# Kernel tuning notes

Hardware: AMD Instinct MI355X
Metric: run time of the kernel (lower is better)

Reference implementation:

```python
import jax, jax.numpy as jnp
import numpy as np

B, N, DPOS, F, P, K = 32, 1024, 3, 64, 128, 16


def setup_inputs() -> dict:
    key = jax.random.key(0)
    kp, kf, kw1, kw2 = jax.random.split(key, 4)
    points = jax.random.normal(kp, (B, N, DPOS), dtype=jnp.float32)
    features = jax.random.normal(kf, (B, N, F), dtype=jnp.float32)
    W1 = jax.random.normal(kw1, (2 * F, 2 * P), dtype=jnp.float32) * (1.0 / np.sqrt(2 * F))
    b1 = jnp.zeros((2 * P,), dtype=jnp.float32)
    W2 = jax.random.normal(kw2, (2 * P, P), dtype=jnp.float32) * (1.0 / np.sqrt(2 * P))
    b2 = jnp.zeros((P,), dtype=jnp.float32)
    return {"points": points, "features": features, "W1": W1, "b1": b1, "W2": W2, "b2": b2}


def reference(points, features, W1, b1, W2, b2):
    # pairwise squared distances: r_i - 2 p_i.p_j + r_j + 1e-5  -> [B, N, N]
    r = jnp.sum(points * points, axis=2, keepdims=True)
    m = jnp.einsum('bnd,bmd->bnm', points, points)
    D = r - 2.0 * m + jnp.swapaxes(r, 1, 2) + 1e-5
    # K+1 nearest (incl. self), drop self -> indices [B, N, K]
    _, idx = jax.lax.top_k(-D, K + 1)
    idx = idx[:, :, 1:]
    # gather neighbor features: [B, N, K, F]
    neighbors = features[jnp.arange(B)[:, None, None], idx]
    center = jnp.broadcast_to(features[:, :, None, :], neighbors.shape)
    local = jnp.concatenate([neighbors - center, center], axis=-1)  # [B,N,K,2F]
    # 2-layer MLP with exact GELU
    h = jax.nn.gelu(jnp.einsum('bnkf,fh->bnkh', local, W1) + b1, approximate=False)
    out = jax.nn.gelu(jnp.einsum('bnkh,hp->bnkp', h, W2) + b2, approximate=False)
    # mean over neighbors -> [B, N, P]
    return jnp.mean(out, axis=2)
```

## Files before the change

kernel.cpp:

```cpp
#include <hip/hip_runtime.h>
#include <math.h>

#define BB 32
#define NN 1024
#define FF 64
#define PP 128
#define KNN 16
#define H2 256
#define F2 128
#define KSEL 17
#define SVCAP 272

typedef float f32x4 __attribute__((ext_vector_type(4)));
typedef _Float16 f16x8 __attribute__((ext_vector_type(8)));

#define GC1 0.39616247f
#define GC3 -0.05891477f
#define GC5 0.00563735f
#define GC7 -2.10439e-4f
#define GXC 3.2988f

__device__ __forceinline__ float gelu_poly(float x) {
    float xc = __builtin_amdgcn_fmed3f(x, -GXC, GXC);
    float s = xc * xc;
    float t = fmaf(s, GC7, GC5);
    t = fmaf(s, t, GC3);
    t = fmaf(s, t, GC1);
    float u = fmaf(xc, t, 0.5f);
    return x * u;
}

__device__ __forceinline__ f16x8 splat8(float f) {
    _Float16 h = (_Float16)f;
    f16x8 v = {h, h, h, h, h, h, h, h};
    return v;
}

__device__ __forceinline__ f16x8 act8(f16x8 gv, f16x8 qv) {
    const f16x8 XL = splat8(-GXC), XH = splat8(GXC);
    const f16x8 C1 = splat8(GC1), C3 = splat8(GC3), C5 = splat8(GC5), C7 = splat8(GC7);
    const f16x8 HF = splat8(0.5f);
    f16x8 x  = gv + qv;
    f16x8 xc = __builtin_elementwise_min(__builtin_elementwise_max(x, XL), XH);
    f16x8 s  = xc * xc;
    f16x8 t  = s * C7 + C5;
    t = s * t + C3;
    t = s * t + C1;
    f16x8 u = xc * t + HF;
    return x * u;
}

__global__ __launch_bounds__(512, 8) void knn_prep(const float* __restrict__ points,
                                                   int* __restrict__ idx_out,
                                                   const float* __restrict__ W1,
                                                   const float* __restrict__ W2,
                                                   _Float16* __restrict__ Wcf,
                                                   _Float16* __restrict__ W2f) {
    if (blockIdx.x >= 4096) {
        int tid = (blockIdx.x - 4096) * 512 + threadIdx.x;
        if (tid < 4096) {
            const int lane = tid & 63, quad = lane >> 4, l16 = lane & 15;
            const int kk = (tid >> 6) & 1, n_tile = tid >> 7;
            const int n = n_tile * 16 + l16;
            const int kb = kk * 32 + quad * 8;
            f16x8 v;
#pragma unroll
            for (int j = 0; j < 8; ++j) {
                const int k = kb + j;
                float x = (n < 256) ? W1[k * 256 + n]
                                    : (W1[(64 + k) * 256 + (n - 256)] - W1[k * 256 + (n - 256)]);
                v[j] = (_Float16)x;
            }
            *(f16x8*)(Wcf + (size_t)tid * 8) = v;
        } else {
            const int t2 = tid - 4096;
            const int lane = t2 & 63, quad = lane >> 4, l16 = lane & 15;
            const int nt = (t2 >> 6) & 7, kk8 = t2 >> 9;
            const int p = nt * 16 + l16;
            const int hb = kk8 * 32 + quad * 8;
            f16x8 v;
#pragma unroll
            for (int j = 0; j < 8; ++j) v[j] = (_Float16)W2[(size_t)(hb + j) * PP + p];
            *(f16x8*)(W2f + (size_t)t2 * 8) = v;
        }
        return;
    }

    __shared__ float px[NN], py[NN], pz[NN], rr[NN];
    __shared__ unsigned sv_val[8][SVCAP];
    __shared__ unsigned sv_idx[8][SVCAP];
    __shared__ unsigned tie_idx[8][64];

    const int t = threadIdx.x;
    const int w = t >> 6, lane = t & 63;
    const int b = blockIdx.x >> 7;
    const int q0 = (blockIdx.x & 127) * 8;
    const float* pb = points + (size_t)b * NN * 3;
    const unsigned long long lt = (1ull << lane) - 1ull;

    for (int i = t; i < NN; i += 512) {
        float x = pb[3 * i], y = pb[3 * i + 1], z = pb[3 * i + 2];
        px[i] = x; py[i] = y; pz[i] = z;
        rr[i] = __fadd_rn(__fadd_rn(__fmul_rn(x, x), __fmul_rn(y, y)), __fmul_rn(z, z));
    }
    __syncthreads();

    const int qn = q0 + w;
    const int gq = b * NN + qn;
    const float qx = px[qn], qy = py[qn], qz = pz[qn], qw = rr[qn];

    float D[16];
#pragma unroll
    for (int j = 0; j < 16; ++j) {
        const int m = j * 64 + lane;
        float dot = __fadd_rn(__fadd_rn(__fmul_rn(qx, px[m]), __fmul_rn(qy, py[m])),
                              __fmul_rn(qz, pz[m]));
        D[j] = __fadd_rn(__fadd_rn(__fsub_rn(qw, __fmul_rn(2.0f, dot)), rr[m]), 1e-5f);
    }

    float mnf = D[0];
#pragma unroll
    for (int j = 1; j < 16; ++j) mnf = fminf(mnf, D[j]);
    const unsigned mbits = __float_as_uint(mnf);

    const unsigned mhi = mbits >> 16;
    unsigned Thi = 0;
#pragma unroll
    for (int bit = 15; bit >= 0; --bit) {
        unsigned cand = Thi | (1u << bit);
        int cnt = __popcll(__ballot(mhi < cand));
        if (cnt < KSEL) Thi = cand;
    }
    const unsigned T = (Thi << 16) | 0xFFFFu;

    unsigned base = 0;
#pragma unroll
    for (int j = 0; j < 16; ++j) {
        unsigned vb = __float_as_uint(D[j]);
        bool keep = (vb <= T);
        unsigned long long m = __ballot(keep);
        if (keep) {
            unsigned pos = base + (unsigned)__popcll(m & lt);
            if (pos < SVCAP) { sv_val[w][pos] = vb; sv_idx[w][pos] = j * 64 + lane; }
        }
        base += (unsigned)__popcll(m);
    }
    unsigned C = base > SVCAP ? SVCAP : base;
    const int S = (int)((C + 63) >> 6);

    unsigned Ts = 0;
    if (S == 1) {
        unsigned xv0 = (lane < (int)C) ? sv_val[w][lane] : 0xFFFFFFFFu;
#pragma unroll
        for (int bit = 31; bit >= 0; --bit) {
            unsigned cand = Ts | (1u << bit);
            int cnt = __popcll(__ballot(xv0 < cand));
            if (cnt < KSEL) Ts = cand;
        }
    } else {
        for (int bit = 31; bit >= 0; --bit) {
            unsigned cand = Ts | (1u << bit);
            int cnt = 0;
            for (int s = 0; s < S; ++s) {
                int i = s * 64 + lane;
                unsigned vb = (i < (int)C) ? sv_val[w][i] : 0xFFFFFFFFu;
                cnt += __popcll(__ballot(vb < cand));
            }
            if (cnt < KSEL) Ts = cand;
        }
    }

    int L = 0;
    for (int s = 0; s < S; ++s) {
        int i = s * 64 + lane;
        unsigned vb = (i < (int)C) ? sv_val[w][i] : 0xFFFFFFFFu;
        L += __popcll(__ballot(vb < Ts));
    }
    const int need = KSEL - L;

    unsigned vmin_l = 0xFFFFFFFFu;
    for (int s = 0; s < S; ++s) {
        int i = s * 64 + lane;
        unsigned vb = (i < (int)C) ? sv_val[w][i] : 0xFFFFFFFFu;
        vmin_l = vmin_l < vb ? vmin_l : vb;
    }
#pragma unroll
    for (int off = 32; off >= 1; off >>= 1) {
        unsigned o2 = __shfl_xor(vmin_l, off, 64);
        vmin_l = vmin_l < o2 ? vmin_l : o2;
    }
    const unsigned Vmin = vmin_l;
    unsigned imin_l = 0xFFFFFFFFu;
    for (int s = 0; s < S; ++s) {
        int i = s * 64 + lane;
        unsigned vb = (i < (int)C) ? sv_val[w][i] : 0xFFFFFFFFu;
        unsigned mi = (i < (int)C) ? sv_idx[w][i] : 0xFFFFFFFFu;
        if (vb == Vmin && mi < imin_l) imin_l = mi;
    }
#pragma unroll
    for (int off = 32; off >= 1; off >>= 1) {
        unsigned o2 = __shfl_xor(imin_l, off, 64);
        imin_l = imin_l < o2 ? imin_l : o2;
    }
    const unsigned dropIdx = imin_l;

    int* o = idx_out + (size_t)gq * KNN;
    unsigned wbase = 0, tbase = 0;
    for (int s = 0; s < S; ++s) {
        int i = s * 64 + lane;
        unsigned vb = (i < (int)C) ? sv_val[w][i] : 0xFFFFFFFFu;
        unsigned mi = (i < (int)C) ? sv_idx[w][i] : 0xFFFFFFFFu;
        bool wk = (vb < Ts) && (mi != dropIdx);
        unsigned long long wm = __ballot(wk);
        if (wk) o[wbase + (unsigned)__popcll(wm & lt)] = (int)mi;
        wbase += (unsigned)__popcll(wm);
        bool tk = (vb == Ts);
        unsigned long long tm2 = __ballot(tk);
        if (tk) {
            unsigned tp = tbase + (unsigned)__popcll(tm2 & lt);
            if (tp < 64) tie_idx[w][tp] = mi;
        }
        tbase += (unsigned)__popcll(tm2);
    }
    unsigned tc = tbase > 64 ? 64 : tbase;
    if ((int)tc == need) {
        bool tk = (lane < (int)tc);
        unsigned mi2 = tk ? tie_idx[w][lane] : 0xFFFFFFFFu;
        tk = tk && (mi2 != dropIdx);
        unsigned long long m3 = __ballot(tk);
        if (tk) o[wbase + (unsigned)__popcll(m3 & lt)] = (int)mi2;
    } else if (lane == 0) {
        unsigned pos = wbase;
        for (int r = 0; r < need; ++r) {
            unsigned best = 0xFFFFFFFFu; int bj = 0;
            for (int j2 = 0; j2 < (int)tc; ++j2) {
                unsigned mi = tie_idx[w][j2];
                if (mi < best) { best = mi; bj = j2; }
            }
            tie_idx[w][bj] = 0xFFFFFFFFu;
            if (best != dropIdx) o[pos++] = (int)best;
        }
    }
}

__global__ __launch_bounds__(256, 4) void gq_gemm(const float* __restrict__ feat,
                                                  const _Float16* __restrict__ Wcf,
                                                  const float* __restrict__ b1,
                                                  _Float16* __restrict__ Gall,
                                                  _Float16* __restrict__ Qall) {
    __shared__ __align__(16) _Float16 st[4][16][136];
    const int t = threadIdx.x, w = t >> 6, lane = t & 63;
    const int quad = lane >> 4, l16 = lane & 15;
    const int m0 = blockIdx.x * 16;

    f16x8 a[2];
#pragma unroll
    for (int kk = 0; kk < 2; ++kk) {
        const float* ap = feat + (size_t)(m0 + l16) * 64 + kk * 32 + quad * 8;
        float4 a0 = *(const float4*)ap, a1 = *(const float4*)(ap + 4);
        f16x8 v;
        v[0] = (_Float16)a0.x; v[1] = (_Float16)a0.y; v[2] = (_Float16)a0.z; v[3] = (_Float16)a0.w;
        v[4] = (_Float16)a1.x; v[5] = (_Float16)a1.y; v[6] = (_Float16)a1.z; v[7] = (_Float16)a1.w;
        a[kk] = v;
    }
    f32x4 acc[8];
#pragma unroll
    for (int nt = 0; nt < 8; ++nt) acc[nt] = (f32x4){0.f, 0.f, 0.f, 0.f};
#pragma unroll
    for (int kk = 0; kk < 2; ++kk)
#pragma unroll
        for (int nt = 0; nt < 8; ++nt) {
            f16x8 bf = *(const f16x8*)(Wcf + (size_t)(((w * 8 + nt) * 2 + kk) * 64 + lane) * 8);
            acc[nt] = __builtin_amdgcn_mfma_f32_16x16x32_f16(a[kk], bf, acc[nt], 0, 0, 0);
        }

    const bool isQ = (w >= 2);
#pragma unroll
    for (int nt = 0; nt < 8; ++nt) {
        const int col = nt * 16 + l16;
        const float bias = isQ ? b1[(w - 2) * 128 + col] : 0.f;
#pragma unroll
        for (int r = 0; r < 4; ++r)
            st[w][quad * 4 + r][col] = (_Float16)(acc[nt][r] + bias);
    }
    __syncthreads();

    const int row = lane >> 2, c = lane & 3;
    const int m = m0 + row;
#pragma unroll
    for (int i = 0; i < 4; ++i) {
        const int col = c * 32 + i * 8;
        f16x8 v = *(const f16x8*)&st[w][row][col];
        if (!isQ) *(f16x8*)(Gall + (size_t)m * H2 + w * 128 + col) = v;
        else      *(f16x8*)(Qall + (size_t)m * H2 + (w - 2) * 128 + col) = v;
    }
}

__global__ __launch_bounds__(512, 4) void fused_mlp10(const _Float16* __restrict__ Gall,
                                                      const _Float16* __restrict__ Qall,
                                                      const int* __restrict__ knn_idx,
                                                      const _Float16* __restrict__ W2f,
                                                      const float* __restrict__ b2,
                                                      float* __restrict__ out) {
    __shared__ __align__(16) _Float16 w2s[16384];
    const int t = threadIdx.x, w = t >> 6, lane = t & 63;
    const int quad = lane >> 4, l16 = lane & 15;

    const int lb = ((blockIdx.x & 7) << 8) | (blockIdx.x >> 3);

    const int q0 = (lb * 8 + w) * 2;
    const int b = q0 >> 10;
    const int nb0 = knn_idx[q0 * KNN + l16];
    const int nb1 = knn_idx[(q0 + 1) * KNN + l16];
    const _Float16* g0 = Gall + ((size_t)(b << 10) + nb0) * H2;
    const _Float16* g1 = Gall + ((size_t)(b << 10) + nb1) * H2;
    const _Float16* qq0 = Qall + (size_t)q0 * H2;
    const _Float16* qq1 = qq0 + H2;

    f32x4 acc[2][8];
#pragma unroll
    for (int tm = 0; tm < 2; ++tm)
#pragma unroll
        for (int nt = 0; nt < 8; ++nt) acc[tm][nt] = (f32x4){0.f, 0.f, 0.f, 0.f};

#pragma unroll
    for (int h = 0; h < 2; ++h) {
        if (h) __syncthreads();
#pragma unroll
        for (int i = 0; i < 4; ++i) {
            f16x8 v = *(const f16x8*)(W2f + (size_t)(h * 16384 + i * 4096 + t * 8));
            *(f16x8*)&w2s[i * 4096 + t * 8] = v;
        }
        __syncthreads();

#pragma unroll
        for (int ql = 0; ql < 2; ++ql)
#pragma unroll
            for (int kl = 0; kl < 2; ++kl) {
                const int ho = (((h * 2 + ql) * 2) + kl) * 32 + quad * 8;
                f16x8 gA = *(const f16x8*)(g0 + ho);
                f16x8 qA = *(const f16x8*)(qq0 + ho);
                f16x8 gB = *(const f16x8*)(g1 + ho);
                f16x8 qB = *(const f16x8*)(qq1 + ho);
                f16x8 a0 = act8(gA, qA);
                f16x8 a1 = act8(gB, qB);
                const _Float16* bb = &w2s[(ql * 2 + kl) * 4096 + lane * 8];
#pragma unroll
                for (int nt = 0; nt < 8; ++nt) {
                    f16x8 bf = *(const f16x8*)(bb + nt * 512);
                    acc[0][nt] = __builtin_amdgcn_mfma_f32_16x16x32_f16(a0, bf, acc[0][nt], 0, 0, 0);
                    acc[1][nt] = __builtin_amdgcn_mfma_f32_16x16x32_f16(a1, bf, acc[1][nt], 0, 0, 0);
                }
            }
    }

    __syncthreads();
    float* obuf = (float*)w2s;
#pragma unroll
    for (int tm = 0; tm < 2; ++tm)
#pragma unroll
        for (int nt = 0; nt < 8; ++nt) {
            const float bias = b2[nt * 16 + l16];
            float s = 0.f;
#pragma unroll
            for (int r = 0; r < 4; ++r) s += gelu_poly(acc[tm][nt][r] + bias);
            s += __shfl_xor(s, 16, 64);
            s += __shfl_xor(s, 32, 64);
            if (quad == 0)
                obuf[(w * 2 + tm) * 128 + nt * 16 + l16] = s * 0.0625f;
        }
    __syncthreads();
    {
        float4 v = *(const float4*)&obuf[t * 4];
        *(float4*)(out + (size_t)lb * 2048 + t * 4) = v;
    }
}

extern "C" void kernel_launch(void* const* d_in, const int* in_sizes, int n_in,
                              void* d_out, int out_size, void* d_ws, size_t ws_size,
                              hipStream_t stream) {
    const float* points   = (const float*)d_in[0];
    const float* features = (const float*)d_in[1];
    const float* W1 = (const float*)d_in[2];
    const float* b1 = (const float*)d_in[3];
    const float* W2 = (const float*)d_in[4];
    const float* b2 = (const float*)d_in[5];
    float* out = (float*)d_out;

    const size_t IDX_B  = (size_t)BB * NN * KNN * 4;
    const size_t WCF_B  = 512 * 64 * 2;
    const size_t W2F_B  = 256 * 128 * 2;
    const size_t G_B    = (size_t)BB * NN * H2 * 2;

    int* knn_idx = (int*)d_ws;
    char* p = (char*)d_ws + IDX_B;
    _Float16* Wcf  = (_Float16*)p;  p += WCF_B;
    _Float16* W2f  = (_Float16*)p;  p += W2F_B;
    _Float16* Gall = (_Float16*)p;  p += G_B;
    _Float16* Qall = (_Float16*)p;

    knn_prep<<<4112, 512, 0, stream>>>(points, knn_idx, W1, W2, Wcf, W2f);
    gq_gemm<<<2048, 256, 0, stream>>>(features, Wcf, b1, Gall, Qall);
    fused_mlp10<<<2048, 512, 0, stream>>>(Gall, Qall, knn_idx, W2f, b2, out);
}
```

Measured before the change: 192.8 us.

## Fuse G/Q projection GEMM into kNN kernel and stage full W2 in LDS

Weight reformatting moves to its own small launch, so the G/Q feature projection can run as extra blocks inside the kNN kernel, which now shares one LDS buffer between both roles. This removes a separate kernel launch and lets the GEMM blocks overlap with the kNN blocks. The MLP kernel now loads all of W2 into 64KB of LDS once instead of in two halves with an extra barrier. The larger LDS footprint may reduce occupancy of the MLP kernel, and the weight prep becomes a serial dependency ahead of the kNN launch.

```diff
diff --git a/kernel.cpp b/kernel.cpp
--- a/kernel.cpp
+++ b/kernel.cpp
@@ -50,48 +50,108 @@
     return x * u;
 }
 
-__global__ __launch_bounds__(512, 8) void knn_prep(const float* __restrict__ points,
-                                                   int* __restrict__ idx_out,
-                                                   const float* __restrict__ W1,
-                                                   const float* __restrict__ W2,
-                                                   _Float16* __restrict__ Wcf,
-                                                   _Float16* __restrict__ W2f) {
+__global__ __launch_bounds__(512) void prep_weights(const float* __restrict__ W1,
+                                                    const float* __restrict__ W2,
+                                                    _Float16* __restrict__ Wcf,
+                                                    _Float16* __restrict__ W2f) {
+    int tid = blockIdx.x * 512 + threadIdx.x;
+    if (tid < 4096) {
+        const int lane = tid & 63, quad = lane >> 4, l16 = lane & 15;
+        const int kk = (tid >> 6) & 1, n_tile = tid >> 7;
+        const int n = n_tile * 16 + l16;
+        const int kb = kk * 32 + quad * 8;
+        f16x8 v;
+#pragma unroll
+        for (int j = 0; j < 8; ++j) {
+            const int k = kb + j;
+            float x = (n < 256) ? W1[k * 256 + n]
+                                : (W1[(64 + k) * 256 + (n - 256)] - W1[k * 256 + (n - 256)]);
+            v[j] = (_Float16)x;
+        }
+        *(f16x8*)(Wcf + (size_t)tid * 8) = v;
+    } else {
+        const int t2 = tid - 4096;
+        const int lane = t2 & 63, quad = lane >> 4, l16 = lane & 15;
+        const int nt = (t2 >> 6) & 7, kk8 = t2 >> 9;
+        const int p = nt * 16 + l16;
+        const int hb = kk8 * 32 + quad * 8;
+        f16x8 v;
+#pragma unroll
+        for (int j = 0; j < 8; ++j) v[j] = (_Float16)W2[(size_t)(hb + j) * PP + p];
+        *(f16x8*)(W2f + (size_t)t2 * 8) = v;
+    }
+}
+
+__global__ __launch_bounds__(512, 8) void knn_gq(const float* __restrict__ points,
+                                                 int* __restrict__ idx_out,
+                                                 const float* __restrict__ feat,
+                                                 const _Float16* __restrict__ Wcf,
+                                                 const float* __restrict__ b1,
+                                                 _Float16* __restrict__ Gall,
+                                                 _Float16* __restrict__ Qall) {
+    __shared__ __align__(16) unsigned char smem[35840];
+    const int t = threadIdx.x;
+
     if (blockIdx.x >= 4096) {
-        int tid = (blockIdx.x - 4096) * 512 + threadIdx.x;
-        if (tid < 4096) {
-            const int lane = tid & 63, quad = lane >> 4, l16 = lane & 15;
-            const int kk = (tid >> 6) & 1, n_tile = tid >> 7;
-            const int n = n_tile * 16 + l16;
-            const int kb = kk * 32 + quad * 8;
+        _Float16 (*st)[16][136] = (_Float16(*)[16][136])smem;
+        const int w8 = t >> 6, lane = t & 63;
+        const int w4 = w8 & 3;
+        const int quad = lane >> 4, l16 = lane & 15;
+        const int gb = blockIdx.x - 4096;
+        const int m0 = gb * 32 + (w8 >> 2) * 16;
+
+        f16x8 a[2];
+#pragma unroll
+        for (int kk = 0; kk < 2; ++kk) {
+            const float* ap = feat + (size_t)(m0 + l16) * 64 + kk * 32 + quad * 8;
+            float4 a0 = *(const float4*)ap, a1 = *(const float4*)(ap + 4);
             f16x8 v;
-#pragma unroll
-            for (int j = 0; j < 8; ++j) {
-                const int k = kb + j;
-                float x = (n < 256) ? W1[k * 256 + n]
-                                    : (W1[(64 + k) * 256 + (n - 256)] - W1[k * 256 + (n - 256)]);
-                v[j] = (_Float16)x;
+            v[0] = (_Float16)a0.x; v[1] = (_Float16)a0.y; v[2] = (_Float16)a0.z; v[3] = (_Float16)a0.w;
+            v[4] = (_Float16)a1.x; v[5] = (_Float16)a1.y; v[6] = (_Float16)a1.z; v[7] = (_Float16)a1.w;
+            a[kk] = v;
+        }
+        f32x4 acc[8];
+#pragma unroll
+        for (int nt = 0; nt < 8; ++nt) acc[nt] = (f32x4){0.f, 0.f, 0.f, 0.f};
+#pragma unroll
+        for (int kk = 0; kk < 2; ++kk)
+#pragma unroll
+            for (int nt = 0; nt < 8; ++nt) {
+                f16x8 bf = *(const f16x8*)(Wcf + (size_t)(((w4 * 8 + nt) * 2 + kk) * 64 + lane) * 8);
+                acc[nt] = __builtin_amdgcn_mfma_f32_16x16x32_f16(a[kk], bf, acc[nt], 0, 0, 0);
             }
-            *(f16x8*)(Wcf + (size_t)tid * 8) = v;
-        } else {
-            const int t2 = tid - 4096;
-            const int lane = t2 & 63, quad = lane >> 4, l16 = lane & 15;
-            const int nt = (t2 >> 6) & 7, kk8 = t2 >> 9;
-            const int p = nt * 16 + l16;
-            const int hb = kk8 * 32 + quad * 8;
-            f16x8 v;
-#pragma unroll
-            for (int j = 0; j < 8; ++j) v[j] = (_Float16)W2[(size_t)(hb + j) * PP + p];
-            *(f16x8*)(W2f + (size_t)t2 * 8) = v;
+
+        const bool isQ = (w4 >= 2);
+#pragma unroll
+        for (int nt = 0; nt < 8; ++nt) {
+            const int col = nt * 16 + l16;
+            const float bias = isQ ? b1[(w4 - 2) * 128 + col] : 0.f;
+#pragma unroll
+            for (int r = 0; r < 4; ++r)
+                st[w8][quad * 4 + r][col] = (_Float16)(acc[nt][r] + bias);
+        }
+        __syncthreads();
+
+        const int row = lane >> 2, c = lane & 3;
+        const int m = m0 + row;
+#pragma unroll
+        for (int i = 0; i < 4; ++i) {
+            const int col = c * 32 + i * 8;
+            f16x8 v = *(const f16x8*)&st[w8][row][col];
+            if (!isQ) *(f16x8*)(Gall + (size_t)m * H2 + w4 * 128 + col) = v;
+            else      *(f16x8*)(Qall + (size_t)m * H2 + (w4 - 2) * 128 + col) = v;
         }
         return;
     }
 
-    __shared__ float px[NN], py[NN], pz[NN], rr[NN];
-    __shared__ unsigned sv_val[8][SVCAP];
-    __shared__ unsigned sv_idx[8][SVCAP];
-    __shared__ unsigned tie_idx[8][64];
-
-    const int t = threadIdx.x;
+    float* px = (float*)smem;
+    float* py = px + NN;
+    float* pz = py + NN;
+    float* rr = pz + NN;
+    unsigned (*sv_val)[SVCAP] = (unsigned(*)[SVCAP])(smem + 16384);
+    unsigned (*sv_idx)[SVCAP] = (unsigned(*)[SVCAP])(smem + 25088);
+    unsigned (*tie_idx)[64]   = (unsigned(*)[64])(smem + 33792);
+
     const int w = t >> 6, lane = t & 63;
     const int b = blockIdx.x >> 7;
     const int q0 = (blockIdx.x & 127) * 8;
@@ -243,72 +303,19 @@
     }
 }
 
-__global__ __launch_bounds__(256, 4) void gq_gemm(const float* __restrict__ feat,
-                                                  const _Float16* __restrict__ Wcf,
-                                                  const float* __restrict__ b1,
-                                                  _Float16* __restrict__ Gall,
-                                                  _Float16* __restrict__ Qall) {
-    __shared__ __align__(16) _Float16 st[4][16][136];
-    const int t = threadIdx.x, w = t >> 6, lane = t & 63;
-    const int quad = lane >> 4, l16 = lane & 15;
-    const int m0 = blockIdx.x * 16;
-
-    f16x8 a[2];
-#pragma unroll
-    for (int kk = 0; kk < 2; ++kk) {
-        const float* ap = feat + (size_t)(m0 + l16) * 64 + kk * 32 + quad * 8;
-        float4 a0 = *(const float4*)ap, a1 = *(const float4*)(ap + 4);
-        f16x8 v;
-        v[0] = (_Float16)a0.x; v[1] = (_Float16)a0.y; v[2] = (_Float16)a0.z; v[3] = (_Float16)a0.w;
-        v[4] = (_Float16)a1.x; v[5] = (_Float16)a1.y; v[6] = (_Float16)a1.z; v[7] = (_Float16)a1.w;
-        a[kk] = v;
-    }
-    f32x4 acc[8];
-#pragma unroll
-    for (int nt = 0; nt < 8; ++nt) acc[nt] = (f32x4){0.f, 0.f, 0.f, 0.f};
-#pragma unroll
-    for (int kk = 0; kk < 2; ++kk)
-#pragma unroll
-        for (int nt = 0; nt < 8; ++nt) {
-            f16x8 bf = *(const f16x8*)(Wcf + (size_t)(((w * 8 + nt) * 2 + kk) * 64 + lane) * 8);
-            acc[nt] = __builtin_amdgcn_mfma_f32_16x16x32_f16(a[kk], bf, acc[nt], 0, 0, 0);
-        }
-
-    const bool isQ = (w >= 2);
-#pragma unroll
-    for (int nt = 0; nt < 8; ++nt) {
-        const int col = nt * 16 + l16;
-        const float bias = isQ ? b1[(w - 2) * 128 + col] : 0.f;
-#pragma unroll
-        for (int r = 0; r < 4; ++r)
-            st[w][quad * 4 + r][col] = (_Float16)(acc[nt][r] + bias);
-    }
-    __syncthreads();
-
-    const int row = lane >> 2, c = lane & 3;
-    const int m = m0 + row;
-#pragma unroll
-    for (int i = 0; i < 4; ++i) {
-        const int col = c * 32 + i * 8;
-        f16x8 v = *(const f16x8*)&st[w][row][col];
-        if (!isQ) *(f16x8*)(Gall + (size_t)m * H2 + w * 128 + col) = v;
-        else      *(f16x8*)(Qall + (size_t)m * H2 + (w - 2) * 128 + col) = v;
-    }
-}
-
-__global__ __launch_bounds__(512, 4) void fused_mlp10(const _Float16* __restrict__ Gall,
+__global__ __launch_bounds__(512, 4) void fused_mlp11(const _Float16* __restrict__ Gall,
                                                       const _Float16* __restrict__ Qall,
                                                       const int* __restrict__ knn_idx,
                                                       const _Float16* __restrict__ W2f,
                                                       const float* __restrict__ b2,
                                                       float* __restrict__ out) {
-    __shared__ __align__(16) _Float16 w2s[16384];
+    __shared__ __align__(16) _Float16 w2s[32768];
     const int t = threadIdx.x, w = t >> 6, lane = t & 63;
     const int quad = lane >> 4, l16 = lane & 15;
 
     const int lb = ((blockIdx.x & 7) << 8) | (blockIdx.x >> 3);
 
-    const int q0 = (lb * 8 + w) * 2;
+    const int q0 = lb * 16 + w * 2;
     const int b = q0 >> 10;
     const int nb0 = knn_idx[q0 * KNN + l16];
     const int nb1 = knn_idx[(q0 + 1) * KNN + l16];
@@ -317,41 +324,36 @@
     const _Float16* qq0 = Qall + (size_t)q0 * H2;
     const _Float16* qq1 = qq0 + H2;
 
+#pragma unroll
+    for (int i = 0; i < 8; ++i) {
+        f16x8 v = *(const f16x8*)(W2f + (size_t)(i * 4096 + t * 8));
+        *(f16x8*)&w2s[i * 4096 + t * 8] = v;
+    }
+
     f32x4 acc[2][8];
 #pragma unroll
     for (int tm = 0; tm < 2; ++tm)
 #pragma unroll
         for (int nt = 0; nt < 8; ++nt) acc[tm][nt] = (f32x4){0.f, 0.f, 0.f, 0.f};
 
-#pragma unroll
-    for (int h = 0; h < 2; ++h) {
-        if (h) __syncthreads();
-#pragma unroll
-        for (int i = 0; i < 4; ++i) {
-            f16x8 v = *(const f16x8*)(W2f + (size_t)(h * 16384 + i * 4096 + t * 8));
-            *(f16x8*)&w2s[i * 4096 + t * 8] = v;
-        }
-        __syncthreads();
-
-#pragma unroll
-        for (int ql = 0; ql < 2; ++ql)
-#pragma unroll
-            for (int kl = 0; kl < 2; ++kl) {
-                const int ho = (((h * 2 + ql) * 2) + kl) * 32 + quad * 8;
-                f16x8 gA = *(const f16x8*)(g0 + ho);
-                f16x8 qA = *(const f16x8*)(qq0 + ho);
-                f16x8 gB = *(const f16x8*)(g1 + ho);
-                f16x8 qB = *(const f16x8*)(qq1 + ho);
-                f16x8 a0 = act8(gA, qA);
-                f16x8 a1 = act8(gB, qB);
-                const _Float16* bb = &w2s[(ql * 2 + kl) * 4096 + lane * 8];
-#pragma unroll
-                for (int nt = 0; nt < 8; ++nt) {
-                    f16x8 bf = *(const f16x8*)(bb + nt * 512);
-                    acc[0][nt] = __builtin_amdgcn_mfma_f32_16x16x32_f16(a0, bf, acc[0][nt], 0, 0, 0);
-                    acc[1][nt] = __builtin_amdgcn_mfma_f32_16x16x32_f16(a1, bf, acc[1][nt], 0, 0, 0);
-                }
-            }
+    __syncthreads();
+
+#pragma unroll
+    for (int rk = 0; rk < 8; ++rk) {
+        const int ho = rk * 32 + quad * 8;
+        f16x8 gA = *(const f16x8*)(g0 + ho);
+        f16x8 qA = *(const f16x8*)(qq0 + ho);
+        f16x8 gB = *(const f16x8*)(g1 + ho);
+        f16x8 qB = *(const f16x8*)(qq1 + ho);
+        f16x8 a0 = act8(gA, qA);
+        f16x8 a1 = act8(gB, qB);
+        const _Float16* bb = &w2s[rk * 4096 + lane * 8];
+#pragma unroll
+        for (int nt = 0; nt < 8; ++nt) {
+            f16x8 bf = *(const f16x8*)(bb + nt * 512);
+            acc[0][nt] = __builtin_amdgcn_mfma_f32_16x16x32_f16(a0, bf, acc[0][nt], 0, 0, 0);
+            acc[1][nt] = __builtin_amdgcn_mfma_f32_16x16x32_f16(a1, bf, acc[1][nt], 0, 0, 0);
+        }
     }
 
     __syncthreads();
@@ -399,7 +401,7 @@
     _Float16* Gall = (_Float16*)p;  p += G_B;
     _Float16* Qall = (_Float16*)p;
 
-    knn_prep<<<4112, 512, 0, stream>>>(points, knn_idx, W1, W2, Wcf, W2f);
-    gq_gemm<<<2048, 256, 0, stream>>>(features, Wcf, b1, Gall, Qall);
-    fused_mlp10<<<2048, 512, 0, stream>>>(Gall, Qall, knn_idx, W2f, b2, out);
-}
+    prep_weights<<<16, 512, 0, stream>>>(W1, W2, Wcf, W2f);
+    knn_gq<<<5120, 512, 0, stream>>>(points, knn_idx, features, Wcf, b1, Gall, Qall);
+    fused_mlp11<<<2048, 512, 0, stream>>>(Gall, Qall, knn_idx, W2f, b2, out);
+}
```

Result: no change. 190.8 us (-1.0%).
